# Kernel optimization log

Measured on AMD Instinct MI355X. Metric: run time of the kernel, lower is better.

Reference implementation:

```python
import jax, jax.numpy as jnp
import numpy as np
from jax import lax

B, S, CIN, COUT = 32, 1024, 256, 256
EPS = 1e-5
LA = 0.1  # ResidualAttention la


def _cnorm(x, w, b):
    # ChannelNorm: mean/var over channel dim (axis=1); torch.var is unbiased (ddof=1)
    m = jnp.mean(x, axis=1, keepdims=True)
    v = jnp.var(x, axis=1, keepdims=True, ddof=1)
    return (x - m) * lax.rsqrt(v + EPS) * w[None, :, None] + b[None, :, None]


def _conv1d(x, w, pad):
    # x: [B, C_in, L], w: [C_out, C_in, K]
    return lax.conv_general_dilated(x, w, (1,), [(pad, pad)],
                                    dimension_numbers=('NCH', 'OIH', 'NCH'))


def _gate(x, fc_w):
    # ResidualAttention: 1x1 conv to 2 classes, mean + la*max over class dim, sigmoid
    y = _conv1d(x, fc_w, 0)                                   # [B, 2, L]
    score = jax.nn.sigmoid(jnp.mean(y, axis=1) + LA * jnp.max(y, axis=1))  # [B, L]
    return x * (1.0 + score[:, None, :])


def _pad_to(x, s):
    # pad_after_conv: zero-pad time dim back to s
    return jnp.pad(x, ((0, 0), (0, 0), (0, s - x.shape[-1])))


def _block(x, cn_w, cn_b, W, pad, fc_w, s):
    h = _conv1d(jax.nn.relu(_cnorm(x, cn_w, cn_b)), W, pad)
    return _pad_to(_gate(h, fc_w), s)


def setup_inputs() -> dict:
    key = jax.random.key(0)
    ks = jax.random.split(key, 8)
    d = {"inputs": jax.random.normal(ks[0], (B, S, CIN), jnp.float32)}
    cins = {4: CIN, 5: COUT, 6: COUT, 7: COUT, 8: COUT}
    for i, k in enumerate(range(4, 9)):
        cin = cins[k]
        d[f"cn{k}_w"] = jnp.ones((cin,), jnp.float32)
        d[f"cn{k}_b"] = jnp.zeros((cin,), jnp.float32)
        d[f"W{k}"] = jax.random.normal(ks[i + 1], (COUT, cin, k), jnp.float32) * (1.0 / np.sqrt(cin * k))
    d["fc_w"] = jax.random.normal(ks[6], (2, COUT, 1), jnp.float32) * (1.0 / np.sqrt(COUT))
    return d


def reference(inputs, cn4_w, cn4_b, W4, cn5_w, cn5_b, W5, cn6_w, cn6_b, W6,
              cn7_w, cn7_b, W7, cn8_w, cn8_b, W8, fc_w):
    x = jnp.transpose(inputs, (0, 2, 1))  # [B, C, S]
    s = x.shape[-1]
    # torch padding: int((k-1)/2) -> k=4:1, k=5:2, k=6:2, k=7:3, k=8:3
    x = _block(x, cn4_w, cn4_b, W4, 1, fc_w, s)
    x = _block(x, cn5_w, cn5_b, W5, 2, fc_w, s)
    x = _block(x, cn6_w, cn6_b, W6, 2, fc_w, s)
    x = _block(x, cn7_w, cn7_b, W7, 3, fc_w, s)
    x = _block(x, cn8_w, cn8_b, W8, 3, fc_w, s)
    return jnp.transpose(x, (0, 2, 1))  # [B, S, C_out]
```

## Files before the change

kernel.cpp:

```cpp
#include <hip/hip_runtime.h>
#include <hip/hip_bf16.h>

#define B_ 32
#define S_ 1024
#define C_ 256
#define SP 1040

typedef float f32x4  __attribute__((ext_vector_type(4)));
typedef float f32x16 __attribute__((ext_vector_type(16)));
typedef __bf16 bf16x8 __attribute__((ext_vector_type(8)));

__global__ __launch_bounds__(256) void wcvt_all(
        const float* __restrict__ w4, const float* __restrict__ w5,
        const float* __restrict__ w6, const float* __restrict__ w7,
        const float* __restrict__ w8, __hip_bfloat16* __restrict__ wb) {
    int i = blockIdx.x * 256 + threadIdx.x;
    const float* src; int base, k;
    if      (i <  262144) { src = w4; base = 0;       k = 4; }
    else if (i <  589824) { src = w5; base = 262144;  k = 5; }
    else if (i <  983040) { src = w6; base = 589824;  k = 6; }
    else if (i < 1441792) { src = w7; base = 983040;  k = 7; }
    else                  { src = w8; base = 1441792; k = 8; }
    int ii = i - base;
    int e = ii & 7, co = (ii >> 3) & 255, hh = (ii >> 11) & 1;
    int ks = (ii >> 12) & 1, c32 = (ii >> 13) & 7, j = ii >> 16;
    int ci = c32 * 32 + ks * 16 + hh * 8 + e;
    wb[i] = __float2bfloat16(src[(co * 256 + ci) * k + j]);
}

__global__ __launch_bounds__(256) void zeroh_kernel(__hip_bfloat16* __restrict__ y) {
    int i = blockIdx.x * 256 + threadIdx.x;
    int b = i >> 9, rr = (i >> 5) & 15, s = i & 31;
    int row = (rr < 8) ? rr : (1024 + rr);
    uint4 z = make_uint4(0, 0, 0, 0);
    *(uint4*)(y + ((size_t)(b * SP + row)) * C_ + s * 8) = z;
}

__global__ __launch_bounds__(256) void prep0_kernel(const float* __restrict__ in,
                                                    const float* __restrict__ cw,
                                                    const float* __restrict__ cb,
                                                    __hip_bfloat16* __restrict__ yout) {
    const int lane = threadIdx.x & 63;
    const int sl   = lane & 31;
    const int rid  = (blockIdx.x * 4 + (threadIdx.x >> 6)) * 2 + (lane >> 5);
    const int b = rid / SP;
    const int t = (rid - b * SP) - 8;
    __hip_bfloat16* drow = yout + (size_t)rid * C_ + sl * 8;
    if (t < 0 || t >= S_) { *(uint4*)drow = make_uint4(0, 0, 0, 0); return; }

    const float* row = in + ((size_t)(b * S_ + t)) * C_ + sl * 8;
    f32x4 x0 = *(const f32x4*)row;
    f32x4 x1 = *(const f32x4*)(row + 4);
    float s1 = x0.x + x0.y + x0.z + x0.w + x1.x + x1.y + x1.z + x1.w;
    float s2 = x0.x*x0.x + x0.y*x0.y + x0.z*x0.z + x0.w*x0.w
             + x1.x*x1.x + x1.y*x1.y + x1.z*x1.z + x1.w*x1.w;
#pragma unroll
    for (int m = 16; m >= 1; m >>= 1) {
        s1 += __shfl_xor(s1, m, 64);
        s2 += __shfl_xor(s2, m, 64);
    }
    float mean = s1 * (1.0f / 256.0f);
    float var  = fmaxf((s2 - 256.0f * mean * mean) * (1.0f / 255.0f), 0.0f);
    float inv  = rsqrtf(var + 1e-5f);
    f32x4 w0 = *(const f32x4*)(cw + sl * 8);
    f32x4 w1 = *(const f32x4*)(cw + sl * 8 + 4);
    f32x4 b0 = *(const f32x4*)(cb + sl * 8);
    f32x4 b1 = *(const f32x4*)(cb + sl * 8 + 4);
    union { uint4 u; __hip_bfloat16 e[8]; } o;
    o.e[0] = __float2bfloat16(fmaxf(0.f, (x0.x - mean)*inv*w0.x + b0.x));
    o.e[1] = __float2bfloat16(fmaxf(0.f, (x0.y - mean)*inv*w0.y + b0.y));
    o.e[2] = __float2bfloat16(fmaxf(0.f, (x0.z - mean)*inv*w0.z + b0.z));
    o.e[3] = __float2bfloat16(fmaxf(0.f, (x0.w - mean)*inv*w0.w + b0.w));
    o.e[4] = __float2bfloat16(fmaxf(0.f, (x1.x - mean)*inv*w1.x + b1.x));
    o.e[5] = __float2bfloat16(fmaxf(0.f, (x1.y - mean)*inv*w1.y + b1.y));
    o.e[6] = __float2bfloat16(fmaxf(0.f, (x1.z - mean)*inv*w1.z + b1.z));
    o.e[7] = __float2bfloat16(fmaxf(0.f, (x1.w - mean)*inv*w1.w + b1.w));
    *(uint4*)drow = o.u;
}

template<int KS, int PAD, int LVALID, bool LAST>
__global__ __launch_bounds__(256, 2) void conv_fused(
        const __hip_bfloat16* __restrict__ y,
        const __hip_bfloat16* __restrict__ wb,
        __hip_bfloat16* __restrict__ ynext,
        float* __restrict__ fout,
        const float* __restrict__ fc,
        const float* __restrict__ cwn,
        const float* __restrict__ cbn) {
    __shared__ alignas(16) __hip_bfloat16 ly[135 * 256];
    __shared__ float redpq[128][4];
    __shared__ float redss[128][4];
    const int tid  = threadIdx.x;
    const int lane = tid & 63;
    const int wv   = tid >> 6;
    const int tt   = blockIdx.x & 7;
    const int b    = blockIdx.x >> 3;
    const int t0   = tt << 7;

    {
        const __hip_bfloat16* yb = y + ((size_t)(b * SP + 8 + t0 - PAD)) * C_;
#pragma unroll
        for (int c = 0; c < 17; ++c) {
            int u = c * 256 + tid;
            if (u < 4320) {
                int r = u >> 5, s2 = u & 31;
                *(bf16x8*)(ly + (size_t)u * 8) =
                    *(const bf16x8*)(yb + (size_t)r * C_ + ((s2 ^ (r & 7)) << 3));
            }
        }
    }
    __syncthreads();

    const int cog = wv & 1;
    const int tq  = wv >> 1;
    const int l31 = lane & 31;
    const int hh  = lane >> 5;

    f32x16 acc[4][2];
#pragma unroll
    for (int mf = 0; mf < 4; ++mf)
#pragma unroll
        for (int nf = 0; nf < 2; ++nf)
#pragma unroll
            for (int e = 0; e < 16; ++e)
                acc[mf][nf][e] = 0.0f;

    const __hip_bfloat16* abase = wb + (size_t)hh * 2048 + (size_t)(cog * 128 + l31) * 8;
    const int rbase = tq * 64 + l31;

    bf16x8 aF[2][2][4], bF[2][2][2];

#define LOADS(ST, S) { \
    const int jj_ = (S) >> 3, cc_ = (S) & 7; \
    _Pragma("unroll") for (int ks = 0; ks < 2; ++ks) { \
        _Pragma("unroll") for (int mf = 0; mf < 4; ++mf) \
            aF[ST][ks][mf] = *(const bf16x8*)(abase + (size_t)((S) * 4 + ks * 2) * 2048 + mf * 256); \
        _Pragma("unroll") for (int nf = 0; nf < 2; ++nf) { \
            int r_ = rbase + nf * 32 + jj_; \
            int ci8_ = cc_ * 4 + ks * 2 + hh; \
            bF[ST][ks][nf] = *(const bf16x8*)(ly + (size_t)r_ * 256 + ((ci8_ ^ (r_ & 7)) << 3)); \
        } } }

#define MM(ST) { \
    _Pragma("unroll") for (int ks = 0; ks < 2; ++ks) \
    _Pragma("unroll") for (int mf = 0; mf < 4; ++mf) \
    _Pragma("unroll") for (int nf = 0; nf < 2; ++nf) \
        acc[mf][nf] = __builtin_amdgcn_mfma_f32_32x32x16_bf16( \
            aF[ST][ks][mf], bF[ST][ks][nf], acc[mf][nf], 0, 0, 0); }

    constexpr int NS = KS * 8;
    LOADS(0, 0)
#pragma unroll 1
    for (int sb = 0; sb < NS / 2 - 1; ++sb) {
        const int s0 = sb * 2;
        LOADS(1, s0 + 1)
        MM(0)
        LOADS(0, s0 + 2)
        MM(1)
    }
    LOADS(1, NS - 1)
    MM(0)
    MM(1)
#undef LOADS
#undef MM

    const int tl0 = tq * 64 + l31, tl1 = tl0 + 32;

    float p0 = 0.f, q0 = 0.f, p1 = 0.f, q1 = 0.f;
#pragma unroll
    for (int mf = 0; mf < 4; ++mf)
#pragma unroll
        for (int r4 = 0; r4 < 4; ++r4) {
            int cb4 = cog * 128 + mf * 32 + r4 * 8 + hh * 4;
            f32x4 f0 = *(const f32x4*)(fc + cb4);
            f32x4 f1 = *(const f32x4*)(fc + 256 + cb4);
#pragma unroll
            for (int qd = 0; qd < 4; ++qd) {
                float a0 = acc[mf][0][r4 * 4 + qd];
                float a1 = acc[mf][1][r4 * 4 + qd];
                p0 += f0[qd] * a0; q0 += f1[qd] * a0;
                p1 += f0[qd] * a1; q1 += f1[qd] * a1;
            }
        }
    p0 += __shfl_xor(p0, 32, 64); q0 += __shfl_xor(q0, 32, 64);
    p1 += __shfl_xor(p1, 32, 64); q1 += __shfl_xor(q1, 32, 64);
    if (!hh) {
        redpq[tl0][cog * 2] = p0; redpq[tl0][cog * 2 + 1] = q0;
        redpq[tl1][cog * 2] = p1; redpq[tl1][cog * 2 + 1] = q1;
    }
    __syncthreads();
    float P0 = p0 + redpq[tl0][(1 - cog) * 2], Q0 = q0 + redpq[tl0][(1 - cog) * 2 + 1];
    float P1 = p1 + redpq[tl1][(1 - cog) * 2], Q1 = q1 + redpq[tl1][(1 - cog) * 2 + 1];
    float sc0 = 0.5f * (P0 + Q0) + 0.1f * fmaxf(P0, Q0);
    float sc1 = 0.5f * (P1 + Q1) + 0.1f * fmaxf(P1, Q1);
    float g0 = 1.0f + 1.0f / (1.0f + expf(-sc0));
    float g1 = 1.0f + 1.0f / (1.0f + expf(-sc1));
    const bool z0 = (LVALID < S_) && (t0 + tl0 >= LVALID);
    const bool z1 = (LVALID < S_) && (t0 + tl1 >= LVALID);

    if constexpr (LAST) {
#pragma unroll
        for (int mf = 0; mf < 4; ++mf)
#pragma unroll
            for (int r4 = 0; r4 < 4; ++r4) {
                int cb4 = cog * 128 + mf * 32 + r4 * 8 + hh * 4;
                f32x4 v0, v1;
#pragma unroll
                for (int qd = 0; qd < 4; ++qd) {
                    v0[qd] = z0 ? 0.0f : acc[mf][0][r4 * 4 + qd] * g0;
                    v1[qd] = z1 ? 0.0f : acc[mf][1][r4 * 4 + qd] * g1;
                }
                *(f32x4*)(fout + ((size_t)(b * S_ + t0 + tl0)) * C_ + cb4) = v0;
                *(f32x4*)(fout + ((size_t)(b * S_ + t0 + tl1)) * C_ + cb4) = v1;
            }
        return;
    }

    float s10 = 0.f, s20 = 0.f, s11 = 0.f, s21 = 0.f;
#pragma unroll
    for (int mf = 0; mf < 4; ++mf)
#pragma unroll
        for (int e = 0; e < 16; ++e) {
            float a0 = acc[mf][0][e] * g0; acc[mf][0][e] = a0; s10 += a0; s20 += a0 * a0;
            float a1 = acc[mf][1][e] * g1; acc[mf][1][e] = a1; s11 += a1; s21 += a1 * a1;
        }
    s10 += __shfl_xor(s10, 32, 64); s20 += __shfl_xor(s20, 32, 64);
    s11 += __shfl_xor(s11, 32, 64); s21 += __shfl_xor(s21, 32, 64);
    if (!hh) {
        redss[tl0][cog * 2] = s10; redss[tl0][cog * 2 + 1] = s20;
        redss[tl1][cog * 2] = s11; redss[tl1][cog * 2 + 1] = s21;
    }
    __syncthreads();
    float S10 = s10 + redss[tl0][(1 - cog) * 2], S20 = s20 + redss[tl0][(1 - cog) * 2 + 1];
    float S11 = s11 + redss[tl1][(1 - cog) * 2], S21 = s21 + redss[tl1][(1 - cog) * 2 + 1];
    float mean0 = S10 * (1.0f / 256.0f);
    float inv0  = rsqrtf(fmaxf((S20 - 256.0f * mean0 * mean0) * (1.0f / 255.0f), 0.0f) + 1e-5f);
    float mean1 = S11 * (1.0f / 256.0f);
    float inv1  = rsqrtf(fmaxf((S21 - 256.0f * mean1 * mean1) * (1.0f / 255.0f), 0.0f) + 1e-5f);

    __hip_bfloat16* yb0 = ynext + ((size_t)(b * SP + 8 + t0 + tl0)) * C_;
    __hip_bfloat16* yb1 = ynext + ((size_t)(b * SP + 8 + t0 + tl1)) * C_;
#pragma unroll
    for (int mf = 0; mf < 4; ++mf)
#pragma unroll
        for (int r4 = 0; r4 < 4; ++r4) {
            int cb4 = cog * 128 + mf * 32 + r4 * 8 + hh * 4;
            f32x4 wv4 = *(const f32x4*)(cwn + cb4);
            f32x4 bv4 = *(const f32x4*)(cbn + cb4);
            union { ushort4 u; __hip_bfloat16 e[4]; } o0, o1;
#pragma unroll
            for (int qd = 0; qd < 4; ++qd) {
                float v0 = z0 ? fmaxf(bv4[qd], 0.f)
                              : fmaxf(0.f, (acc[mf][0][r4 * 4 + qd] - mean0) * inv0 * wv4[qd] + bv4[qd]);
                float v1 = z1 ? fmaxf(bv4[qd], 0.f)
                              : fmaxf(0.f, (acc[mf][1][r4 * 4 + qd] - mean1) * inv1 * wv4[qd] + bv4[qd]);
                o0.e[qd] = __float2bfloat16(v0);
                o1.e[qd] = __float2bfloat16(v1);
            }
            *(ushort4*)(yb0 + cb4) = o0.u;
            *(ushort4*)(yb1 + cb4) = o1.u;
        }
}

extern "C" void kernel_launch(void* const* d_in, const int* in_sizes, int n_in,
                              void* d_out, int out_size, void* d_ws, size_t ws_size,
                              hipStream_t stream) {
    const float* inputs = (const float*)d_in[0];
    const float* cw[5] = { (const float*)d_in[1],  (const float*)d_in[4],
                           (const float*)d_in[7],  (const float*)d_in[10],
                           (const float*)d_in[13] };
    const float* cb[5] = { (const float*)d_in[2],  (const float*)d_in[5],
                           (const float*)d_in[8],  (const float*)d_in[11],
                           (const float*)d_in[14] };
    const float* Wf[5] = { (const float*)d_in[3],  (const float*)d_in[6],
                           (const float*)d_in[9],  (const float*)d_in[12],
                           (const float*)d_in[15] };
    const float* fc = (const float*)d_in[16];

    char* ws = (char*)d_ws;
    __hip_bfloat16* yP = (__hip_bfloat16*)ws;
    __hip_bfloat16* yQ = (__hip_bfloat16*)(ws + 17039360);
    __hip_bfloat16* wb = (__hip_bfloat16*)(ws + 34078720);
    float* out = (float*)d_out;

    wcvt_all<<<7680, 256, 0, stream>>>(Wf[0], Wf[1], Wf[2], Wf[3], Wf[4], wb);
    zeroh_kernel<<<64, 256, 0, stream>>>(yQ);
    prep0_kernel<<<4160, 256, 0, stream>>>(inputs, cw[0], cb[0], yP);

    conv_fused<4, 1, 1023, false><<<256, 256, 0, stream>>>(yP, wb,           yQ, nullptr, fc, cw[1], cb[1]);
    conv_fused<5, 2, 1024, false><<<256, 256, 0, stream>>>(yQ, wb +  262144, yP, nullptr, fc, cw[2], cb[2]);
    conv_fused<6, 2, 1023, false><<<256, 256, 0, stream>>>(yP, wb +  589824, yQ, nullptr, fc, cw[3], cb[3]);
    conv_fused<7, 3, 1024, false><<<256, 256, 0, stream>>>(yQ, wb +  983040, yP, nullptr, fc, cw[4], cb[4]);
    conv_fused<8, 3, 1023, true ><<<256, 256, 0, stream>>>(yP, wb + 1441792, nullptr, out, fc, nullptr, nullptr);
}
```

Before: 383.4 us.

## Shrink conv tiles to 32 timesteps and stage output stores through LDS

Each block now computes 32 timesteps across all 256 output channels, with each of the 4 waves owning 64 channels, instead of 128 timesteps split over a 2x2 wave grid. This gives 1024 blocks instead of 256, which fills the 256 CUs better and raises occupancy via smaller LDS and fewer accumulators. Output writes are staged through LDS so that global stores are coalesced full rows. The trade-off is less weight reuse per block, so each weight fragment is reloaded from global/L2 four times as often, plus a larger fraction of halo rows.

New measurement: 310.6 us. 19.0% less time.

```diff
diff --git a/kernel.cpp b/kernel.cpp
--- a/kernel.cpp
+++ b/kernel.cpp
@@ -79,7 +79,7 @@
 }
 
 template<int KS, int PAD, int LVALID, bool LAST>
-__global__ __launch_bounds__(256, 2) void conv_fused(
+__global__ __launch_bounds__(256, 4) void conv_fused(
         const __hip_bfloat16* __restrict__ y,
         const __hip_bfloat16* __restrict__ wb,
         __hip_bfloat16* __restrict__ ynext,
@@ -87,22 +87,26 @@
         const float* __restrict__ fc,
         const float* __restrict__ cwn,
         const float* __restrict__ cbn) {
-    __shared__ alignas(16) __hip_bfloat16 ly[135 * 256];
-    __shared__ float redpq[128][4];
-    __shared__ float redss[128][4];
+    __shared__ alignas(16) __hip_bfloat16 ly[39 * 256];
+    __shared__ float redpq[4][32][2];
+    __shared__ float redss[4][32][2];
     const int tid  = threadIdx.x;
     const int lane = tid & 63;
-    const int wv   = tid >> 6;
-    const int tt   = blockIdx.x & 7;
-    const int b    = blockIdx.x >> 3;
-    const int t0   = tt << 7;
-
+    const int cog  = tid >> 6;
+    const int tt   = blockIdx.x & 31;
+    const int b    = blockIdx.x >> 5;
+    const int t0   = tt << 5;
+    const int l31  = lane & 31;
+    const int hh   = lane >> 5;
+
+    constexpr int RSTG  = 32 + KS - 1;
+    constexpr int UNITS = RSTG * 32;
     {
         const __hip_bfloat16* yb = y + ((size_t)(b * SP + 8 + t0 - PAD)) * C_;
 #pragma unroll
-        for (int c = 0; c < 17; ++c) {
+        for (int c = 0; c < (UNITS + 255) / 256; ++c) {
             int u = c * 256 + tid;
-            if (u < 4320) {
+            if (u < UNITS) {
                 int r = u >> 5, s2 = u & 31;
                 *(bf16x8*)(ly + (size_t)u * 8) =
                     *(const bf16x8*)(yb + (size_t)r * C_ + ((s2 ^ (r & 7)) << 3));
@@ -111,42 +115,32 @@
     }
     __syncthreads();
 
-    const int cog = wv & 1;
-    const int tq  = wv >> 1;
-    const int l31 = lane & 31;
-    const int hh  = lane >> 5;
-
-    f32x16 acc[4][2];
-#pragma unroll
-    for (int mf = 0; mf < 4; ++mf)
-#pragma unroll
-        for (int nf = 0; nf < 2; ++nf)
-#pragma unroll
-            for (int e = 0; e < 16; ++e)
-                acc[mf][nf][e] = 0.0f;
-
-    const __hip_bfloat16* abase = wb + (size_t)hh * 2048 + (size_t)(cog * 128 + l31) * 8;
-    const int rbase = tq * 64 + l31;
-
-    bf16x8 aF[2][2][4], bF[2][2][2];
+    f32x16 acc[2];
+#pragma unroll
+    for (int mf = 0; mf < 2; ++mf)
+#pragma unroll
+        for (int e = 0; e < 16; ++e)
+            acc[mf][e] = 0.0f;
+
+    const __hip_bfloat16* abase = wb + (size_t)hh * 2048 + (size_t)(cog * 64 + l31) * 8;
+
+    bf16x8 aF[2][2][2], bF[2][2];
 
 #define LOADS(ST, S) { \
     const int jj_ = (S) >> 3, cc_ = (S) & 7; \
     _Pragma("unroll") for (int ks = 0; ks < 2; ++ks) { \
-        _Pragma("unroll") for (int mf = 0; mf < 4; ++mf) \
+        _Pragma("unroll") for (int mf = 0; mf < 2; ++mf) \
             aF[ST][ks][mf] = *(const bf16x8*)(abase + (size_t)((S) * 4 + ks * 2) * 2048 + mf * 256); \
-        _Pragma("unroll") for (int nf = 0; nf < 2; ++nf) { \
-            int r_ = rbase + nf * 32 + jj_; \
-            int ci8_ = cc_ * 4 + ks * 2 + hh; \
-            bF[ST][ks][nf] = *(const bf16x8*)(ly + (size_t)r_ * 256 + ((ci8_ ^ (r_ & 7)) << 3)); \
-        } } }
+        { int r_ = l31 + jj_; \
+          int ci8_ = cc_ * 4 + ks * 2 + hh; \
+          bF[ST][ks] = *(const bf16x8*)(ly + (size_t)r_ * 256 + ((ci8_ ^ (r_ & 7)) << 3)); } \
+    } }
 
 #define MM(ST) { \
     _Pragma("unroll") for (int ks = 0; ks < 2; ++ks) \
-    _Pragma("unroll") for (int mf = 0; mf < 4; ++mf) \
-    _Pragma("unroll") for (int nf = 0; nf < 2; ++nf) \
-        acc[mf][nf] = __builtin_amdgcn_mfma_f32_32x32x16_bf16( \
-            aF[ST][ks][mf], bF[ST][ks][nf], acc[mf][nf], 0, 0, 0); }
+    _Pragma("unroll") for (int mf = 0; mf < 2; ++mf) \
+        acc[mf] = __builtin_amdgcn_mfma_f32_32x32x16_bf16( \
+            aF[ST][ks][mf], bF[ST][ks], acc[mf], 0, 0, 0); }
 
     constexpr int NS = KS * 8;
     LOADS(0, 0)
@@ -164,102 +158,102 @@
 #undef LOADS
 #undef MM
 
-    const int tl0 = tq * 64 + l31, tl1 = tl0 + 32;
-
-    float p0 = 0.f, q0 = 0.f, p1 = 0.f, q1 = 0.f;
-#pragma unroll
-    for (int mf = 0; mf < 4; ++mf)
+    const int t = l31;
+
+    float p = 0.f, q = 0.f;
+#pragma unroll
+    for (int mf = 0; mf < 2; ++mf)
 #pragma unroll
         for (int r4 = 0; r4 < 4; ++r4) {
-            int cb4 = cog * 128 + mf * 32 + r4 * 8 + hh * 4;
+            int cb4 = cog * 64 + mf * 32 + r4 * 8 + hh * 4;
             f32x4 f0 = *(const f32x4*)(fc + cb4);
             f32x4 f1 = *(const f32x4*)(fc + 256 + cb4);
 #pragma unroll
             for (int qd = 0; qd < 4; ++qd) {
-                float a0 = acc[mf][0][r4 * 4 + qd];
-                float a1 = acc[mf][1][r4 * 4 + qd];
-                p0 += f0[qd] * a0; q0 += f1[qd] * a0;
-                p1 += f0[qd] * a1; q1 += f1[qd] * a1;
-            }
-        }
-    p0 += __shfl_xor(p0, 32, 64); q0 += __shfl_xor(q0, 32, 64);
-    p1 += __shfl_xor(p1, 32, 64); q1 += __shfl_xor(q1, 32, 64);
-    if (!hh) {
-        redpq[tl0][cog * 2] = p0; redpq[tl0][cog * 2 + 1] = q0;
-        redpq[tl1][cog * 2] = p1; redpq[tl1][cog * 2 + 1] = q1;
-    }
-    __syncthreads();
-    float P0 = p0 + redpq[tl0][(1 - cog) * 2], Q0 = q0 + redpq[tl0][(1 - cog) * 2 + 1];
-    float P1 = p1 + redpq[tl1][(1 - cog) * 2], Q1 = q1 + redpq[tl1][(1 - cog) * 2 + 1];
-    float sc0 = 0.5f * (P0 + Q0) + 0.1f * fmaxf(P0, Q0);
-    float sc1 = 0.5f * (P1 + Q1) + 0.1f * fmaxf(P1, Q1);
-    float g0 = 1.0f + 1.0f / (1.0f + expf(-sc0));
-    float g1 = 1.0f + 1.0f / (1.0f + expf(-sc1));
-    const bool z0 = (LVALID < S_) && (t0 + tl0 >= LVALID);
-    const bool z1 = (LVALID < S_) && (t0 + tl1 >= LVALID);
+                float a = acc[mf][r4 * 4 + qd];
+                p += f0[qd] * a; q += f1[qd] * a;
+            }
+        }
+    p += __shfl_xor(p, 32, 64); q += __shfl_xor(q, 32, 64);
+    if (!hh) { redpq[cog][t][0] = p; redpq[cog][t][1] = q; }
+    __syncthreads();
+    float P = redpq[0][t][0] + redpq[1][t][0] + redpq[2][t][0] + redpq[3][t][0];
+    float Q = redpq[0][t][1] + redpq[1][t][1] + redpq[2][t][1] + redpq[3][t][1];
+    float sc = 0.5f * (P + Q) + 0.1f * fmaxf(P, Q);
+    float g  = 1.0f + 1.0f / (1.0f + expf(-sc));
+    const bool z = (LVALID < S_) && (t0 + t >= LVALID);
 
     if constexpr (LAST) {
-#pragma unroll
-        for (int mf = 0; mf < 4; ++mf)
-#pragma unroll
-            for (int r4 = 0; r4 < 4; ++r4) {
-                int cb4 = cog * 128 + mf * 32 + r4 * 8 + hh * 4;
-                f32x4 v0, v1;
-#pragma unroll
-                for (int qd = 0; qd < 4; ++qd) {
-                    v0[qd] = z0 ? 0.0f : acc[mf][0][r4 * 4 + qd] * g0;
-                    v1[qd] = z1 ? 0.0f : acc[mf][1][r4 * 4 + qd] * g1;
-                }
-                *(f32x4*)(fout + ((size_t)(b * S_ + t0 + tl0)) * C_ + cb4) = v0;
-                *(f32x4*)(fout + ((size_t)(b * S_ + t0 + tl1)) * C_ + cb4) = v1;
-            }
+        float* lof = (float*)ly;
+#pragma unroll
+        for (int pass = 0; pass < 2; ++pass) {
+            __syncthreads();
+            if ((t >> 4) == pass) {
+                int rr = t & 15;
+#pragma unroll
+                for (int mf = 0; mf < 2; ++mf)
+#pragma unroll
+                    for (int r4 = 0; r4 < 4; ++r4) {
+                        int cb4 = cog * 64 + mf * 32 + r4 * 8 + hh * 4;
+                        f32x4 v;
+#pragma unroll
+                        for (int qd = 0; qd < 4; ++qd)
+                            v[qd] = z ? 0.0f : acc[mf][r4 * 4 + qd] * g;
+                        *(f32x4*)(lof + rr * 260 + cb4) = v;
+                    }
+            }
+            __syncthreads();
+#pragma unroll
+            for (int c = 0; c < 4; ++c) {
+                int u = c * 256 + tid;
+                int row = u >> 6, c4 = u & 63;
+                *(f32x4*)(fout + ((size_t)(b * S_ + t0 + pass * 16 + row)) * C_ + c4 * 4) =
+                    *(const f32x4*)(lof + row * 260 + c4 * 4);
+            }
+        }
         return;
     }
 
-    float s10 = 0.f, s20 = 0.f, s11 = 0.f, s21 = 0.f;
-#pragma unroll
-    for (int mf = 0; mf < 4; ++mf)
+    float s1 = 0.f, s2 = 0.f;
+#pragma unroll
+    for (int mf = 0; mf < 2; ++mf)
 #pragma unroll
         for (int e = 0; e < 16; ++e) {
-            float a0 = acc[mf][0][e] * g0; acc[mf][0][e] = a0; s10 += a0; s20 += a0 * a0;
-            float a1 = acc[mf][1][e] * g1; acc[mf][1][e] = a1; s11 += a1; s21 += a1 * a1;
-        }
-    s10 += __shfl_xor(s10, 32, 64); s20 += __shfl_xor(s20, 32, 64);
-    s11 += __shfl_xor(s11, 32, 64); s21 += __shfl_xor(s21, 32, 64);
-    if (!hh) {
-        redss[tl0][cog * 2] = s10; redss[tl0][cog * 2 + 1] = s20;
-        redss[tl1][cog * 2] = s11; redss[tl1][cog * 2 + 1] = s21;
-    }
-    __syncthreads();
-    float S10 = s10 + redss[tl0][(1 - cog) * 2], S20 = s20 + redss[tl0][(1 - cog) * 2 + 1];
-    float S11 = s11 + redss[tl1][(1 - cog) * 2], S21 = s21 + redss[tl1][(1 - cog) * 2 + 1];
-    float mean0 = S10 * (1.0f / 256.0f);
-    float inv0  = rsqrtf(fmaxf((S20 - 256.0f * mean0 * mean0) * (1.0f / 255.0f), 0.0f) + 1e-5f);
-    float mean1 = S11 * (1.0f / 256.0f);
-    float inv1  = rsqrtf(fmaxf((S21 - 256.0f * mean1 * mean1) * (1.0f / 255.0f), 0.0f) + 1e-5f);
-
-    __hip_bfloat16* yb0 = ynext + ((size_t)(b * SP + 8 + t0 + tl0)) * C_;
-    __hip_bfloat16* yb1 = ynext + ((size_t)(b * SP + 8 + t0 + tl1)) * C_;
-#pragma unroll
-    for (int mf = 0; mf < 4; ++mf)
+            float a = acc[mf][e] * g; acc[mf][e] = a; s1 += a; s2 += a * a;
+        }
+    s1 += __shfl_xor(s1, 32, 64); s2 += __shfl_xor(s2, 32, 64);
+    if (!hh) { redss[cog][t][0] = s1; redss[cog][t][1] = s2; }
+    __syncthreads();
+    float S1 = redss[0][t][0] + redss[1][t][0] + redss[2][t][0] + redss[3][t][0];
+    float S2 = redss[0][t][1] + redss[1][t][1] + redss[2][t][1] + redss[3][t][1];
+    float mean = S1 * (1.0f / 256.0f);
+    float inv  = rsqrtf(fmaxf((S2 - 256.0f * mean * mean) * (1.0f / 255.0f), 0.0f) + 1e-5f);
+
+    __hip_bfloat16* lo = ly;
+#pragma unroll
+    for (int mf = 0; mf < 2; ++mf)
 #pragma unroll
         for (int r4 = 0; r4 < 4; ++r4) {
-            int cb4 = cog * 128 + mf * 32 + r4 * 8 + hh * 4;
+            int cb4 = cog * 64 + mf * 32 + r4 * 8 + hh * 4;
             f32x4 wv4 = *(const f32x4*)(cwn + cb4);
             f32x4 bv4 = *(const f32x4*)(cbn + cb4);
-            union { ushort4 u; __hip_bfloat16 e[4]; } o0, o1;
+            union { ushort4 u; __hip_bfloat16 e[4]; } o;
 #pragma unroll
             for (int qd = 0; qd < 4; ++qd) {
-                float v0 = z0 ? fmaxf(bv4[qd], 0.f)
-                              : fmaxf(0.f, (acc[mf][0][r4 * 4 + qd] - mean0) * inv0 * wv4[qd] + bv4[qd]);
-                float v1 = z1 ? fmaxf(bv4[qd], 0.f)
-                              : fmaxf(0.f, (acc[mf][1][r4 * 4 + qd] - mean1) * inv1 * wv4[qd] + bv4[qd]);
-                o0.e[qd] = __float2bfloat16(v0);
-                o1.e[qd] = __float2bfloat16(v1);
-            }
-            *(ushort4*)(yb0 + cb4) = o0.u;
-            *(ushort4*)(yb1 + cb4) = o1.u;
-        }
+                float v = z ? fmaxf(bv4[qd], 0.f)
+                            : fmaxf(0.f, (acc[mf][r4 * 4 + qd] - mean) * inv * wv4[qd] + bv4[qd]);
+                o.e[qd] = __float2bfloat16(v);
+            }
+            *(ushort4*)(lo + t * 264 + cb4) = o.u;
+        }
+    __syncthreads();
+#pragma unroll
+    for (int c = 0; c < 4; ++c) {
+        int u = c * 256 + tid;
+        int row = u >> 5, c16 = u & 31;
+        *(bf16x8*)(ynext + ((size_t)(b * SP + 8 + t0 + row)) * C_ + c16 * 8) =
+            *(const bf16x8*)(lo + row * 264 + c16 * 8);
+    }
 }
 
 extern "C" void kernel_launch(void* const* d_in, const int* in_sizes, int n_in,
@@ -287,9 +281,9 @@
     zeroh_kernel<<<64, 256, 0, stream>>>(yQ);
     prep0_kernel<<<4160, 256, 0, stream>>>(inputs, cw[0], cb[0], yP);
 
-    conv_fused<4, 1, 1023, false><<<256, 256, 0, stream>>>(yP, wb,           yQ, nullptr, fc, cw[1], cb[1]);
-    conv_fused<5, 2, 1024, false><<<256, 256, 0, stream>>>(yQ, wb +  262144, yP, nullptr, fc, cw[2], cb[2]);
-    conv_fused<6, 2, 1023, false><<<256, 256, 0, stream>>>(yP, wb +  589824, yQ, nullptr, fc, cw[3], cb[3]);
-    conv_fused<7, 3, 1024, false><<<256, 256, 0, stream>>>(yQ, wb +  983040, yP, nullptr, fc, cw[4], cb[4]);
-    conv_fused<8, 3, 1023, true ><<<256, 256, 0, stream>>>(yP, wb + 1441792, nullptr, out, fc, nullptr, nullptr);
-}
+    conv_fused<4, 1, 1023, false><<<1024, 256, 0, stream>>>(yP, wb,           yQ, nullptr, fc, cw[1], cb[1]);
+    conv_fused<5, 2, 1024, false><<<1024, 256, 0, stream>>>(yQ, wb +  262144, yP, nullptr, fc, cw[2], cb[2]);
+    conv_fused<6, 2, 1023, false><<<1024, 256, 0, stream>>>(yP, wb +  589824, yQ, nullptr, fc, cw[3], cb[3]);
+    conv_fused<7, 3, 1024, false><<<1024, 256, 0, stream>>>(yQ, wb +  983040, yP, nullptr, fc, cw[4], cb[4]);
+    conv_fused<8, 3, 1023, true ><<<1024, 256, 0, stream>>>(yP, wb + 1441792, nullptr, out, fc, nullptr, nullptr);
+}
```
